# Kernel optimization log

Measured on AMD Instinct MI355X. Metric: run time of the kernel, lower is better.

Reference implementation:

```python
import jax, jax.numpy as jnp
import numpy as np

D_MODEL, H, D_FF = 1024, 16, 4096
D_K = D_MODEL // H
EPS = 1e-5


def _layernorm(x, alpha, bias):
    # faithful to source: unbiased std (ddof=1), eps added to std (not var)
    mean = jnp.mean(x, axis=-1, keepdims=True)
    std = jnp.std(x, axis=-1, keepdims=True, ddof=1)
    return alpha * (x - mean) / (std + EPS) + bias


def setup_inputs() -> dict:
    key = jax.random.key(0)
    ks = jax.random.split(key, 12)
    B, S = 2, 2048
    s = 1.0 / np.sqrt(D_MODEL)
    inp = {
        "x": jax.random.normal(ks[0], (B, S, D_MODEL), dtype=jnp.float32),
        "mask": jnp.ones((B, 1, 1, S), dtype=jnp.int32),
        "wq": jax.random.normal(ks[1], (D_MODEL, D_MODEL), dtype=jnp.float32) * s,
        "wk": jax.random.normal(ks[2], (D_MODEL, D_MODEL), dtype=jnp.float32) * s,
        "wv": jax.random.normal(ks[3], (D_MODEL, D_MODEL), dtype=jnp.float32) * s,
        "wo": jax.random.normal(ks[4], (D_MODEL, D_MODEL), dtype=jnp.float32) * s,
        "w1": jax.random.normal(ks[5], (D_MODEL, D_FF), dtype=jnp.float32) * s,
        "b1": jnp.zeros((D_FF,), dtype=jnp.float32),
        "w2": jax.random.normal(ks[6], (D_FF, D_MODEL), dtype=jnp.float32) * (1.0 / np.sqrt(D_FF)),
        "b2": jnp.zeros((D_MODEL,), dtype=jnp.float32),
        "alpha1": jnp.ones((1,), dtype=jnp.float32),
        "bias1": jnp.zeros((1,), dtype=jnp.float32),
        "alpha2": jnp.ones((1,), dtype=jnp.float32),
        "bias2": jnp.zeros((1,), dtype=jnp.float32),
    }
    return inp


def reference(x, mask, wq, wk, wv, wo, w1, b1, w2, b2, alpha1, bias1, alpha2, bias2):
    B, S, _ = x.shape

    # --- sublayer 1: pre-norm self-attention + residual ---
    xn = _layernorm(x, alpha1, bias1)
    q = (xn @ wq).reshape(B, S, H, D_K).transpose(0, 2, 1, 3)  # [B,H,S,Dk]
    k = (xn @ wk).reshape(B, S, H, D_K).transpose(0, 2, 1, 3)
    v = (xn @ wv).reshape(B, S, H, D_K).transpose(0, 2, 1, 3)

    scores = jnp.einsum("bhqd,bhkd->bhqk", q, k) / np.sqrt(D_K)  # [B,H,S,S]
    scores = jnp.where(mask == 0, jnp.float32(-1e9), scores)
    attn = jax.nn.softmax(scores, axis=-1)
    ctx = jnp.einsum("bhqk,bhkd->bhqd", attn, v)
    ctx = ctx.transpose(0, 2, 1, 3).reshape(B, S, D_MODEL)
    x = x + ctx @ wo

    # --- sublayer 2: pre-norm FFN + residual ---
    xn = _layernorm(x, alpha2, bias2)
    h = jax.nn.relu(xn @ w1 + b1)
    x = x + h @ w2 + b2
    return x
```

## Files before the change

### kernel.cpp

```cpp
#include <hip/hip_runtime.h>
#include <hip/hip_bf16.h>

typedef __attribute__((ext_vector_type(8))) short bf16x8;
typedef __attribute__((ext_vector_type(4))) short short4v;
typedef __attribute__((ext_vector_type(4))) float floatx4;

#define MFMA16(A, B, C) __builtin_amdgcn_mfma_f32_16x16x32_bf16((A), (B), (C), 0, 0, 0)

__device__ inline short bf16bits(float f) {
  __hip_bfloat16 h = __float2bfloat16(f);
  return *reinterpret_cast<short*>(&h);
}
__device__ inline unsigned cvtpk(float lo, float hi) {
  unsigned r;
  asm("v_cvt_pk_bf16_f32 %0, %1, %2" : "=v"(r) : "v"(lo), "v"(hi));
  return r;
}
typedef __attribute__((address_space(3))) char lds_char;
typedef __attribute__((address_space(1))) const char glob_char;
__device__ inline void gll16(const void* g, void* l) {
  __builtin_amdgcn_global_load_lds((glob_char*)g, (lds_char*)l, 16, 0, 0);
}

__global__ __launch_bounds__(256) void transpose_f2b_kernel(
    const float* __restrict__ src, __hip_bfloat16* __restrict__ dst,
    int R, int C, int ldS) {
  __shared__ __align__(16) __hip_bfloat16 tile[64][72];
  const long r0 = (long)blockIdx.y * 64, c0 = (long)blockIdx.x * 64;
  for (int i = threadIdx.x; i < 1024; i += 256) {
    int r = i >> 4, c4 = (i & 15) * 4;
    float4 f = *(const float4*)&src[(r0 + r) * ldS + c0 + c4];
    short4v s;
    s[0] = bf16bits(f.x); s[1] = bf16bits(f.y);
    s[2] = bf16bits(f.z); s[3] = bf16bits(f.w);
    *(short4v*)&tile[r][c4] = s;
  }
  __syncthreads();
  for (int i = threadIdx.x; i < 512; i += 256) {
    int c = i >> 3, r8 = (i & 7) * 8;
    bf16x8 sv;
#pragma unroll
    for (int j = 0; j < 8; j++) sv[j] = *reinterpret_cast<const short*>(&tile[r8 + j][c]);
    *(bf16x8*)&dst[(c0 + c) * R + r0 + r8] = sv;
  }
}

__global__ __launch_bounds__(256) void transpose_qkv_kernel(
    const float* __restrict__ wq, const float* __restrict__ wk,
    const float* __restrict__ wv, __hip_bfloat16* __restrict__ wqkvT) {
  __shared__ __align__(16) __hip_bfloat16 tile[64][72];
  const int which = blockIdx.y >> 4;
  const float* src = which == 0 ? wq : (which == 1 ? wk : wv);
  __hip_bfloat16* dst = wqkvT + (size_t)which * 1024 * 1024;
  const long r0 = (long)(blockIdx.y & 15) * 64, c0 = (long)blockIdx.x * 64;
  for (int i = threadIdx.x; i < 1024; i += 256) {
    int r = i >> 4, c4 = (i & 15) * 4;
    float4 f = *(const float4*)&src[(r0 + r) * 1024 + c0 + c4];
    short4v s;
    s[0] = bf16bits(f.x); s[1] = bf16bits(f.y);
    s[2] = bf16bits(f.z); s[3] = bf16bits(f.w);
    *(short4v*)&tile[r][c4] = s;
  }
  __syncthreads();
  for (int i = threadIdx.x; i < 512; i += 256) {
    int c = i >> 3, r8 = (i & 7) * 8;
    bf16x8 sv;
#pragma unroll
    for (int j = 0; j < 8; j++) sv[j] = *reinterpret_cast<const short*>(&tile[r8 + j][c]);
    *(bf16x8*)&dst[(c0 + c) * 1024 + r0 + r8] = sv;
  }
}

__global__ __launch_bounds__(256) void vtrans_kernel(
    const __hip_bfloat16* __restrict__ qkv, __hip_bfloat16* __restrict__ vt) {
  __shared__ __align__(16) __hip_bfloat16 tile[64][72];
  const int bh = blockIdx.y, b = bh >> 4, h = bh & 15;
  const long s0 = (long)blockIdx.x * 64;
  const __hip_bfloat16* src = qkv + ((long)b * 2048 + s0) * 3072 + 2048 + h * 64;
  for (int i = threadIdx.x; i < 512; i += 256) {
    int s = i >> 3, d8 = (i & 7) * 8;
    *(uint4*)&tile[s][d8] = *(const uint4*)&src[(long)s * 3072 + d8];
  }
  __syncthreads();
  __hip_bfloat16* dstb = vt + (long)bh * 64 * 2048 + s0;
  for (int i = threadIdx.x; i < 512; i += 256) {
    int d = i >> 3, s8 = (i & 7) * 8;
    bf16x8 sv;
#pragma unroll
    for (int j = 0; j < 8; j++) sv[j] = *reinterpret_cast<const short*>(&tile[s8 + j][d]);
    *(bf16x8*)&dstb[(long)d * 2048 + s8] = sv;
  }
}

__global__ __launch_bounds__(256) void mask2add_kernel(
    const int* __restrict__ mask, float* __restrict__ addm,
    int* __restrict__ flags) {
  const int i = blockIdx.x * 256 + threadIdx.x;
  const int mv = mask[i];
  addm[i] = mv ? 0.f : -1e30f;
  __shared__ int ok[4];
  const unsigned long long bal = __ballot(mv != 0);
  if ((threadIdx.x & 63) == 0) ok[threadIdx.x >> 6] = (bal == ~0ull) ? 1 : 0;
  __syncthreads();
  if (threadIdx.x == 0) flags[blockIdx.x] = ok[0] & ok[1] & ok[2] & ok[3];
}

__global__ __launch_bounds__(256) void bias_add_kernel(
    const float* __restrict__ x1, const float* __restrict__ b2,
    float* __restrict__ out) {
  const int i = (blockIdx.x * 256 + threadIdx.x) * 4;
  float4 v = *(const float4*)&x1[i];
  const float4 bb = *(const float4*)&b2[i & 1023];
  v.x += bb.x; v.y += bb.y; v.z += bb.z; v.w += bb.w;
  *(float4*)&out[i] = v;
}

__global__ __launch_bounds__(256) void ln_kernel(
    const float* __restrict__ x, __hip_bfloat16* __restrict__ y,
    const float* __restrict__ alpha_p, const float* __restrict__ bias_p) {
  __shared__ float sred[8];
  const long row = blockIdx.x;
  const int t = threadIdx.x;
  const float* xr = x + row * 1024;
  float v[4];
#pragma unroll
  for (int i = 0; i < 4; i++) v[i] = xr[t * 4 + i];
  float sum = 0.f, sq = 0.f;
#pragma unroll
  for (int i = 0; i < 4; i++) { sum += v[i]; sq += v[i] * v[i]; }
#pragma unroll
  for (int off = 32; off; off >>= 1) {
    sum += __shfl_down(sum, off);
    sq += __shfl_down(sq, off);
  }
  if ((t & 63) == 0) { sred[(t >> 6) * 2] = sum; sred[(t >> 6) * 2 + 1] = sq; }
  __syncthreads();
  sum = sred[0] + sred[2] + sred[4] + sred[6];
  sq = sred[1] + sred[3] + sred[5] + sred[7];
  const float mean = sum * (1.f / 1024.f);
  float var = (sq - 1024.f * mean * mean) * (1.f / 1023.f);
  var = fmaxf(var, 0.f);
  const float denom = sqrtf(var) + 1e-5f;
  const float sc = alpha_p[0] / denom;
  const float beta = bias_p[0];
  __hip_bfloat16* yr = y + row * 1024;
#pragma unroll
  for (int i = 0; i < 4; i++) yr[t * 4 + i] = __float2bfloat16((v[i] - mean) * sc + beta);
}

template <int EPI>
__global__ __launch_bounds__(256) void gemm_bt_kernel(
    const __hip_bfloat16* __restrict__ A, const __hip_bfloat16* __restrict__ Bt,
    void* __restrict__ Cv, const float* __restrict__ bias,
    const float* __restrict__ res, int M, int N, int K) {
  __shared__ __align__(16) __hip_bfloat16 lA[128 * 32];
  __shared__ __align__(16) __hip_bfloat16 lB[128 * 32];
  const int tid = threadIdx.x;
  const int wave = tid >> 6, lane = tid & 63;
  const int quad = lane >> 4, l16 = lane & 15;
  const int wm = wave >> 1, wn = wave & 1;
  const long m0 = (long)blockIdx.y * 128;
  const long n0 = (long)blockIdx.x * 128;

  const int rA0 = tid >> 2, cA0 = (tid & 3) * 8;
  const int rA1 = (tid + 256) >> 2, cA1 = ((tid + 256) & 3) * 8;

  floatx4 acc[4][4];
#pragma unroll
  for (int i = 0; i < 4; i++)
#pragma unroll
    for (int j = 0; j < 4; j++) acc[i][j] = (floatx4){0.f, 0.f, 0.f, 0.f};

  const __hip_bfloat16* Ab = A + m0 * K;
  const __hip_bfloat16* Bb = Bt + n0 * K;

  for (int k0 = 0; k0 < K; k0 += 32) {
    __syncthreads();
    gll16(&Ab[(long)rA0 * K + k0 + cA0], &lA[wave * 512]);
    gll16(&Ab[(long)rA1 * K + k0 + cA1], &lA[2048 + wave * 512]);
    gll16(&Bb[(long)rA0 * K + k0 + cA0], &lB[wave * 512]);
    gll16(&Bb[(long)rA1 * K + k0 + cA1], &lB[2048 + wave * 512]);
    __syncthreads();
    bf16x8 af[4], bfr[4];
#pragma unroll
    for (int mi = 0; mi < 4; mi++)
      af[mi] = *(const bf16x8*)&lA[(wm * 64 + mi * 16 + l16) * 32 + quad * 8];
#pragma unroll
    for (int ni = 0; ni < 4; ni++)
      bfr[ni] = *(const bf16x8*)&lB[(wn * 64 + ni * 16 + l16) * 32 + quad * 8];
#pragma unroll
    for (int mi = 0; mi < 4; mi++)
#pragma unroll
      for (int ni = 0; ni < 4; ni++)
        acc[mi][ni] = MFMA16(af[mi], bfr[ni], acc[mi][ni]);
  }

#pragma unroll
  for (int mi = 0; mi < 4; mi++) {
#pragma unroll
    for (int ni = 0; ni < 4; ni++) {
#pragma unroll
      for (int r = 0; r < 4; r++) {
        const long row = m0 + wm * 64 + mi * 16 + quad * 4 + r;
        const long col = n0 + wn * 64 + ni * 16 + l16;
        const long idx = row * N + col;
        float v = acc[mi][ni][r];
        if (EPI == 0) {
          ((__hip_bfloat16*)Cv)[idx] = __float2bfloat16(v);
        } else if (EPI == 1) {
          ((float*)Cv)[idx] = v + res[idx];
        } else if (EPI == 2) {
          v += bias[col];
          ((__hip_bfloat16*)Cv)[idx] = __float2bfloat16(fmaxf(v, 0.f));
        } else if (EPI == 3) {
          float* Cf = (float*)Cv;
          Cf[idx] = Cf[idx] + v;
        }
      }
    }
  }
}

template <int EPI>
__global__ __launch_bounds__(256) void gemm64_bt_kernel(
    const __hip_bfloat16* __restrict__ A, const __hip_bfloat16* __restrict__ Bt,
    void* __restrict__ Cv, const float* __restrict__ bias,
    const float* __restrict__ res, int M, int N, int K) {
  __shared__ __align__(16) __hip_bfloat16 lA[128 * 32];
  __shared__ __align__(16) __hip_bfloat16 lB[64 * 32];
  const int tid = threadIdx.x;
  const int wave = tid >> 6, lane = tid & 63;
  const int quad = lane >> 4, l16 = lane & 15;
  const int wm = wave >> 1, wn = wave & 1;
  const long m0 = (long)blockIdx.y * 128;
  const long n0 = (long)blockIdx.x * 64;

  const int rA0 = tid >> 2, cA0 = (tid & 3) * 8;
  const int rA1 = (tid + 256) >> 2, cA1 = ((tid + 256) & 3) * 8;

  floatx4 acc[4][2];
#pragma unroll
  for (int i = 0; i < 4; i++)
#pragma unroll
    for (int j = 0; j < 2; j++) acc[i][j] = (floatx4){0.f, 0.f, 0.f, 0.f};

  const __hip_bfloat16* Ab = A + m0 * K;
  const __hip_bfloat16* Bb = Bt + n0 * K;

  for (int k0 = 0; k0 < K; k0 += 32) {
    __syncthreads();
    gll16(&Ab[(long)rA0 * K + k0 + cA0], &lA[wave * 512]);
    gll16(&Ab[(long)rA1 * K + k0 + cA1], &lA[2048 + wave * 512]);
    gll16(&Bb[(long)rA0 * K + k0 + cA0], &lB[wave * 512]);
    __syncthreads();
    bf16x8 af[4], bfr[2];
#pragma unroll
    for (int mi = 0; mi < 4; mi++)
      af[mi] = *(const bf16x8*)&lA[(wm * 64 + mi * 16 + l16) * 32 + quad * 8];
#pragma unroll
    for (int ni = 0; ni < 2; ni++)
      bfr[ni] = *(const bf16x8*)&lB[(wn * 32 + ni * 16 + l16) * 32 + quad * 8];
#pragma unroll
    for (int mi = 0; mi < 4; mi++)
#pragma unroll
      for (int ni = 0; ni < 2; ni++)
        acc[mi][ni] = MFMA16(af[mi], bfr[ni], acc[mi][ni]);
  }

#pragma unroll
  for (int mi = 0; mi < 4; mi++) {
#pragma unroll
    for (int ni = 0; ni < 2; ni++) {
#pragma unroll
      for (int r = 0; r < 4; r++) {
        const long row = m0 + wm * 64 + mi * 16 + quad * 4 + r;
        const long col = n0 + wn * 32 + ni * 16 + l16;
        const long idx = row * N + col;
        float v = acc[mi][ni][r];
        if (EPI == 1) {
          ((float*)Cv)[idx] = v + res[idx];
        } else if (EPI == 3) {
          float* Cf = (float*)Cv;
          Cf[idx] = Cf[idx] + v;
        }
      }
    }
  }
}

__global__ __launch_bounds__(256) void attn_kernel(
    const __hip_bfloat16* __restrict__ qkv, const __hip_bfloat16* __restrict__ vt,
    const float* __restrict__ addm, const int* __restrict__ flags,
    __hip_bfloat16* __restrict__ ctx) {
  __shared__ __align__(16) __hip_bfloat16 lK[2][64 * 64];
  __shared__ __align__(16) __hip_bfloat16 lV[2][64 * 64];
  const int tid = threadIdx.x, wave = tid >> 6, lane = tid & 63;
  const int quad = lane >> 4, l16 = lane & 15;
  const int bh = blockIdx.y, b = bh >> 4, h = bh & 15;
  const int q0 = blockIdx.x * 64 + wave * 16;
  const float cs = 0.18033688011112042f;
  const float inv_cs = 5.545177444479562f;

  const __hip_bfloat16* kb = qkv + (long)b * 2048 * 3072 + 1024 + h * 64;
  const __hip_bfloat16* vb = vt + (long)bh * 64 * 2048;
  const float* am = addm + b * 2048;

  int fm = 1;
#pragma unroll
  for (int i = 0; i < 8; ++i) fm &= flags[b * 8 + i];
  const bool fast = (fm != 0);

  const long qoff = ((long)b * 2048 + q0 + l16) * 3072 + h * 64;
  const bf16x8 bq0 = *(const bf16x8*)&qkv[qoff + quad * 8];
  const bf16x8 bq1 = *(const bf16x8*)&qkv[qoff + 32 + quad * 8];

  const int srow = lane >> 3;
  const int cslot = lane & 7;
  const int cg = cslot ^ srow;
  const int rbase = wave * 16 + srow;

  floatx4 o[4];
#pragma unroll
  for (int mi = 0; mi < 4; mi++) o[mi] = (floatx4){0.f, 0.f, 0.f, 0.f};
  float mrow = 10.0f, lrow = 0.f;

#pragma unroll
  for (int j = 0; j < 2; ++j) {
    const int rloc = rbase + j * 8;
    gll16(kb + (long)rloc * 3072 + cg * 8, &lK[0][(wave * 16 + j * 8) * 64]);
    gll16(vb + (long)rloc * 2048 + cg * 8, &lV[0][(wave * 16 + j * 8) * 64]);
  }

  int cur = 0;
  for (int t = 0; t < 32; ++t) {
    __syncthreads();
    if (t + 1 < 32) {
      const int nxt = cur ^ 1;
#pragma unroll
      for (int j = 0; j < 2; ++j) {
        const int rloc = rbase + j * 8;
        gll16(kb + (long)((t + 1) * 64 + rloc) * 3072 + cg * 8,
              &lK[nxt][(wave * 16 + j * 8) * 64]);
        gll16(vb + (long)rloc * 2048 + (t + 1) * 64 + cg * 8,
              &lV[nxt][(wave * 16 + j * 8) * 64]);
      }
    }
    const __hip_bfloat16* lKc = lK[cur];
    const __hip_bfloat16* lVc = lV[cur];

    floatx4 c[4];
    __builtin_amdgcn_s_setprio(1);
#pragma unroll
    for (int g = 0; g < 4; ++g) {
      const bf16x8 a0 =
          *(const bf16x8*)&lKc[(g * 16 + l16) * 64 + ((quad) ^ (l16 & 7)) * 8];
      const bf16x8 a1 =
          *(const bf16x8*)&lKc[(g * 16 + l16) * 64 + ((4 + quad) ^ (l16 & 7)) * 8];
      floatx4 cc = {0.f, 0.f, 0.f, 0.f};
      cc = MFMA16(a0, bq0, cc);
      cc = MFMA16(a1, bq1, cc);
      c[g] = cc;
    }
    __builtin_amdgcn_s_setprio(0);

    if (!fast) {
#pragma unroll
      for (int g = 0; g < 4; ++g) {
        const float4 a4 = *(const float4*)&am[t * 64 + g * 16 + quad * 4];
        c[g][0] = fmaf(a4.x, inv_cs, c[g][0]);
        c[g][1] = fmaf(a4.y, inv_cs, c[g][1]);
        c[g][2] = fmaf(a4.z, inv_cs, c[g][2]);
        c[g][3] = fmaf(a4.w, inv_cs, c[g][3]);
      }
    }

    const float mneg = -mrow;
    float p[4][4];
#pragma unroll
    for (int g = 0; g < 4; ++g)
#pragma unroll
      for (int r = 0; r < 4; ++r)
        p[g][r] = __builtin_amdgcn_exp2f(fmaf(c[g][r], cs, mneg));

    const float m0 = fmaxf(fmaxf(c[0][0], c[0][1]), c[0][2]);
    const float m1 = fmaxf(fmaxf(c[0][3], c[1][0]), c[1][1]);
    const float m2 = fmaxf(fmaxf(c[1][2], c[1][3]), c[2][0]);
    const float m3 = fmaxf(fmaxf(c[2][1], c[2][2]), c[2][3]);
    const float m4 = fmaxf(fmaxf(c[3][0], c[3][1]), c[3][2]);
    float tm = fmaxf(fmaxf(fmaxf(m0, m1), fmaxf(m2, m3)), fmaxf(m4, c[3][3]));
    tm = fmaxf(tm, __shfl_xor(tm, 16));
    tm = fmaxf(tm, __shfl_xor(tm, 32));
    const float tms = tm * cs;

    const float s0 = (p[0][0] + p[0][1]) + (p[0][2] + p[0][3]);
    const float s1 = (p[1][0] + p[1][1]) + (p[1][2] + p[1][3]);
    const float s2 = (p[2][0] + p[2][1]) + (p[2][2] + p[2][3]);
    const float s3 = (p[3][0] + p[3][1]) + (p[3][2] + p[3][3]);
    float rs = (s0 + s1) + (s2 + s3);
    rs += __shfl_xor(rs, 16);
    rs += __shfl_xor(rs, 32);

    unsigned dw[4][2];
#pragma unroll
    for (int g = 0; g < 4; ++g) {
      dw[g][0] = cvtpk(p[g][0], p[g][1]);
      dw[g][1] = cvtpk(p[g][2], p[g][3]);
    }
    const int qs0 = (quad & 1) * 2;
    const int src0 = l16 + 16 * qs0, src1 = src0 + 16;
    const bool hig = (quad >> 1) != 0;
#pragma unroll
    for (int ss = 0; ss < 2; ++ss) {
      const unsigned a0 = __shfl((int)dw[2 * ss][0], src0);
      const unsigned b0 = __shfl((int)dw[2 * ss + 1][0], src0);
      const unsigned a1 = __shfl((int)dw[2 * ss][1], src0);
      const unsigned b1 = __shfl((int)dw[2 * ss + 1][1], src0);
      const unsigned a2 = __shfl((int)dw[2 * ss][0], src1);
      const unsigned b2 = __shfl((int)dw[2 * ss + 1][0], src1);
      const unsigned a3 = __shfl((int)dw[2 * ss][1], src1);
      const unsigned b3 = __shfl((int)dw[2 * ss + 1][1], src1);
      uint4 du;
      du.x = hig ? b0 : a0;
      du.y = hig ? b1 : a1;
      du.z = hig ? b2 : a2;
      du.w = hig ? b3 : a3;
      const bf16x8 bp = *reinterpret_cast<bf16x8*>(&du);
      __builtin_amdgcn_s_setprio(1);
#pragma unroll
      for (int mi = 0; mi < 4; ++mi) {
        const bf16x8 av = *(const bf16x8*)&lVc[(mi * 16 + l16) * 64 +
                                               ((ss * 4 + quad) ^ (l16 & 7)) * 8];
        o[mi] = MFMA16(av, bp, o[mi]);
      }
      __builtin_amdgcn_s_setprio(0);
    }

    lrow += rs;
    if (__any(tms > mrow + 8.f)) {
      const float mnew = fmaxf(mrow, tms);
      const float alpha = __builtin_amdgcn_exp2f(mrow - mnew);
      mrow = mnew;
      lrow *= alpha;
#pragma unroll
      for (int mi = 0; mi < 4; mi++) o[mi] *= alpha;
    }
    cur ^= 1;
  }

  const float inv_l = 1.f / lrow;
  const long cb = ((long)b * 2048 + q0 + l16) * 1024 + h * 64;
#pragma unroll
  for (int mi = 0; mi < 4; mi++) {
    uint2 st;
    st.x = cvtpk(o[mi][0] * inv_l, o[mi][1] * inv_l);
    st.y = cvtpk(o[mi][2] * inv_l, o[mi][3] * inv_l);
    *(uint2*)&ctx[cb + mi * 16 + quad * 4] = st;
  }
}

extern "C" void kernel_launch(void* const* d_in, const int* in_sizes, int n_in,
                              void* d_out, int out_size, void* d_ws, size_t ws_size,
                              hipStream_t stream) {
  const float* x = (const float*)d_in[0];
  const int* mask = (const int*)d_in[1];
  const float* wq = (const float*)d_in[2];
  const float* wk = (const float*)d_in[3];
  const float* wv = (const float*)d_in[4];
  const float* wo = (const float*)d_in[5];
  const float* w1 = (const float*)d_in[6];
  const float* b1 = (const float*)d_in[7];
  const float* w2 = (const float*)d_in[8];
  const float* b2 = (const float*)d_in[9];
  const float* alpha1 = (const float*)d_in[10];
  const float* bias1 = (const float*)d_in[11];
  const float* alpha2 = (const float*)d_in[12];
  const float* bias2 = (const float*)d_in[13];

  char* ws = (char*)d_ws;
  char* dob = (char*)d_out;
  const size_t MiB = 1048576;
  __hip_bfloat16* qkv   = (__hip_bfloat16*)(ws + 0);
  __hip_bfloat16* wqkvT = (__hip_bfloat16*)(ws + 24 * MiB);
  __hip_bfloat16* vtb   = (__hip_bfloat16*)(ws + 24 * MiB);
  float*          x1    = (float*)(ws + 0);
  __hip_bfloat16* hc    = (__hip_bfloat16*)(ws + 16 * MiB);
  __hip_bfloat16* xn    = (__hip_bfloat16*)d_out;
  __hip_bfloat16* ctxb  = (__hip_bfloat16*)d_out;
  __hip_bfloat16* xn2   = (__hip_bfloat16*)d_out;
  __hip_bfloat16* woT   = (__hip_bfloat16*)(dob + 8 * MiB);
  __hip_bfloat16* w1Th  = (__hip_bfloat16*)(dob + 8 * MiB);
  __hip_bfloat16* w2Th  = (__hip_bfloat16*)(dob + 12 * MiB);
  float*          addm  = (float*)(dob + 12 * MiB);
  int*            flags = (int*)(dob + 12 * MiB + 16 * 1024);

  const dim3 b256(256);
  const dim3 g1k(16, 16);
  transpose_qkv_kernel<<<dim3(16, 48), b256, 0, stream>>>(wq, wk, wv, wqkvT);
  ln_kernel<<<4096, b256, 0, stream>>>(x, xn, alpha1, bias1);
  gemm_bt_kernel<0><<<dim3(24, 32), b256, 0, stream>>>(xn, wqkvT, qkv, nullptr, nullptr,
                                                       4096, 3072, 1024);
  vtrans_kernel<<<dim3(32, 32), b256, 0, stream>>>(qkv, vtb);
  mask2add_kernel<<<16, b256, 0, stream>>>(mask, addm, flags);
  attn_kernel<<<dim3(32, 32), b256, 0, stream>>>(qkv, vtb, addm, flags, ctxb);
  transpose_f2b_kernel<<<g1k, b256, 0, stream>>>(wo, woT, 1024, 1024, 1024);
  gemm64_bt_kernel<1><<<dim3(16, 32), b256, 0, stream>>>(ctxb, woT, x1, nullptr, x,
                                                         4096, 1024, 1024);
  ln_kernel<<<4096, b256, 0, stream>>>(x1, xn2, alpha2, bias2);
  for (int c = 0; c < 2; ++c) {
    transpose_f2b_kernel<<<dim3(32, 16), b256, 0, stream>>>(w1 + c * 2048, w1Th,
                                                            1024, 2048, 4096);
    gemm_bt_kernel<2><<<dim3(16, 32), b256, 0, stream>>>(xn2, w1Th, hc, b1 + c * 2048,
                                                         nullptr, 4096, 2048, 1024);
    transpose_f2b_kernel<<<dim3(16, 32), b256, 0, stream>>>(w2 + (size_t)c * 2048 * 1024,
                                                            w2Th, 2048, 1024, 1024);
    gemm64_bt_kernel<3><<<dim3(16, 32), b256, 0, stream>>>(hc, w2Th, x1, nullptr,
                                                           nullptr, 4096, 1024, 2048);
  }
  bias_add_kernel<<<4096, b256, 0, stream>>>(x1, b2, (float*)d_out);
}
```

Measured before the change: 458.3 us.

## Double-buffer LDS tiles in GEMM kernels and remap workgroups across XCDs

Both bf16 GEMM kernels now keep two LDS buffers per operand. The global-to-LDS loads for the next K-step are issued before the MFMAs on the current step, which drops one barrier per iteration and lets memory traffic overlap compute. Block IDs are also remapped in strides of 8 so that consecutive tiles share L2 within an XCD. The cost is double the LDS footprint, which may lower occupancy, and the compiler may still insert full vmcnt waits that serialise the async loads. The remap also assumes the workgroup count is divisible by 8.

```diff
diff --git a/kernel.cpp b/kernel.cpp
--- a/kernel.cpp
+++ b/kernel.cpp
@@ -153,14 +153,19 @@
     const __hip_bfloat16* __restrict__ A, const __hip_bfloat16* __restrict__ Bt,
     void* __restrict__ Cv, const float* __restrict__ bias,
     const float* __restrict__ res, int M, int N, int K) {
-  __shared__ __align__(16) __hip_bfloat16 lA[128 * 32];
-  __shared__ __align__(16) __hip_bfloat16 lB[128 * 32];
+  __shared__ __align__(16) __hip_bfloat16 lA[2][128 * 32];
+  __shared__ __align__(16) __hip_bfloat16 lB[2][128 * 32];
   const int tid = threadIdx.x;
   const int wave = tid >> 6, lane = tid & 63;
   const int quad = lane >> 4, l16 = lane & 15;
   const int wm = wave >> 1, wn = wave & 1;
-  const long m0 = (long)blockIdx.y * 128;
-  const long n0 = (long)blockIdx.x * 128;
+
+  const int gx = gridDim.x;
+  const int nwg = gx * gridDim.y;
+  int bid = blockIdx.y * gx + blockIdx.x;
+  bid = (bid & 7) * (nwg >> 3) + (bid >> 3);
+  const long m0 = (long)(bid / gx) * 128;
+  const long n0 = (long)(bid % gx) * 128;
 
   const int rA0 = tid >> 2, cA0 = (tid & 3) * 8;
   const int rA1 = (tid + 256) >> 2, cA1 = ((tid + 256) & 3) * 8;
@@ -174,25 +179,34 @@
   const __hip_bfloat16* Ab = A + m0 * K;
   const __hip_bfloat16* Bb = Bt + n0 * K;
 
+  gll16(&Ab[(long)rA0 * K + cA0], &lA[0][wave * 512]);
+  gll16(&Ab[(long)rA1 * K + cA1], &lA[0][2048 + wave * 512]);
+  gll16(&Bb[(long)rA0 * K + cA0], &lB[0][wave * 512]);
+  gll16(&Bb[(long)rA1 * K + cA1], &lB[0][2048 + wave * 512]);
+
+  int cur = 0;
   for (int k0 = 0; k0 < K; k0 += 32) {
     __syncthreads();
-    gll16(&Ab[(long)rA0 * K + k0 + cA0], &lA[wave * 512]);
-    gll16(&Ab[(long)rA1 * K + k0 + cA1], &lA[2048 + wave * 512]);
-    gll16(&Bb[(long)rA0 * K + k0 + cA0], &lB[wave * 512]);
-    gll16(&Bb[(long)rA1 * K + k0 + cA1], &lB[2048 + wave * 512]);
-    __syncthreads();
+    if (k0 + 32 < K) {
+      const int nxt = cur ^ 1;
+      gll16(&Ab[(long)rA0 * K + k0 + 32 + cA0], &lA[nxt][wave * 512]);
+      gll16(&Ab[(long)rA1 * K + k0 + 32 + cA1], &lA[nxt][2048 + wave * 512]);
+      gll16(&Bb[(long)rA0 * K + k0 + 32 + cA0], &lB[nxt][wave * 512]);
+      gll16(&Bb[(long)rA1 * K + k0 + 32 + cA1], &lB[nxt][2048 + wave * 512]);
+    }
     bf16x8 af[4], bfr[4];
 #pragma unroll
     for (int mi = 0; mi < 4; mi++)
-      af[mi] = *(const bf16x8*)&lA[(wm * 64 + mi * 16 + l16) * 32 + quad * 8];
+      af[mi] = *(const bf16x8*)&lA[cur][(wm * 64 + mi * 16 + l16) * 32 + quad * 8];
 #pragma unroll
     for (int ni = 0; ni < 4; ni++)
-      bfr[ni] = *(const bf16x8*)&lB[(wn * 64 + ni * 16 + l16) * 32 + quad * 8];
+      bfr[ni] = *(const bf16x8*)&lB[cur][(wn * 64 + ni * 16 + l16) * 32 + quad * 8];
 #pragma unroll
     for (int mi = 0; mi < 4; mi++)
 #pragma unroll
       for (int ni = 0; ni < 4; ni++)
         acc[mi][ni] = MFMA16(af[mi], bfr[ni], acc[mi][ni]);
+    cur ^= 1;
   }
 
 #pragma unroll
@@ -226,14 +240,19 @@
     const __hip_bfloat16* __restrict__ A, const __hip_bfloat16* __restrict__ Bt,
     void* __restrict__ Cv, const float* __restrict__ bias,
     const float* __restrict__ res, int M, int N, int K) {
-  __shared__ __align__(16) __hip_bfloat16 lA[128 * 32];
-  __shared__ __align__(16) __hip_bfloat16 lB[64 * 32];
+  __shared__ __align__(16) __hip_bfloat16 lA[2][128 * 32];
+  __shared__ __align__(16) __hip_bfloat16 lB[2][64 * 32];
   const int tid = threadIdx.x;
   const int wave = tid >> 6, lane = tid & 63;
   const int quad = lane >> 4, l16 = lane & 15;
   const int wm = wave >> 1, wn = wave & 1;
-  const long m0 = (long)blockIdx.y * 128;
-  const long n0 = (long)blockIdx.x * 64;
+
+  const int gx = gridDim.x;
+  const int nwg = gx * gridDim.y;
+  int bid = blockIdx.y * gx + blockIdx.x;
+  bid = (bid & 7) * (nwg >> 3) + (bid >> 3);
+  const long m0 = (long)(bid / gx) * 128;
+  const long n0 = (long)(bid % gx) * 64;
 
   const int rA0 = tid >> 2, cA0 = (tid & 3) * 8;
   const int rA1 = (tid + 256) >> 2, cA1 = ((tid + 256) & 3) * 8;
@@ -247,24 +266,32 @@
   const __hip_bfloat16* Ab = A + m0 * K;
   const __hip_bfloat16* Bb = Bt + n0 * K;
 
+  gll16(&Ab[(long)rA0 * K + cA0], &lA[0][wave * 512]);
+  gll16(&Ab[(long)rA1 * K + cA1], &lA[0][2048 + wave * 512]);
+  gll16(&Bb[(long)rA0 * K + cA0], &lB[0][wave * 512]);
+
+  int cur = 0;
   for (int k0 = 0; k0 < K; k0 += 32) {
     __syncthreads();
-    gll16(&Ab[(long)rA0 * K + k0 + cA0], &lA[wave * 512]);
-    gll16(&Ab[(long)rA1 * K + k0 + cA1], &lA[2048 + wave * 512]);
-    gll16(&Bb[(long)rA0 * K + k0 + cA0], &lB[wave * 512]);
-    __syncthreads();
+    if (k0 + 32 < K) {
+      const int nxt = cur ^ 1;
+      gll16(&Ab[(long)rA0 * K + k0 + 32 + cA0], &lA[nxt][wave * 512]);
+      gll16(&Ab[(long)rA1 * K + k0 + 32 + cA1], &lA[nxt][2048 + wave * 512]);
+      gll16(&Bb[(long)rA0 * K + k0 + 32 + cA0], &lB[nxt][wave * 512]);
+    }
     bf16x8 af[4], bfr[2];
 #pragma unroll
     for (int mi = 0; mi < 4; mi++)
-      af[mi] = *(const bf16x8*)&lA[(wm * 64 + mi * 16 + l16) * 32 + quad * 8];
+      af[mi] = *(const bf16x8*)&lA[cur][(wm * 64 + mi * 16 + l16) * 32 + quad * 8];
 #pragma unroll
     for (int ni = 0; ni < 2; ni++)
-      bfr[ni] = *(const bf16x8*)&lB[(wn * 32 + ni * 16 + l16) * 32 + quad * 8];
+      bfr[ni] = *(const bf16x8*)&lB[cur][(wn * 32 + ni * 16 + l16) * 32 + quad * 8];
 #pragma unroll
     for (int mi = 0; mi < 4; mi++)
 #pragma unroll
       for (int ni = 0; ni < 2; ni++)
         acc[mi][ni] = MFMA16(af[mi], bfr[ni], acc[mi][ni]);
+    cur ^= 1;
   }
 
 #pragma unroll
```

Result: faster. 438.2 us (-4.4%).
